# Optimization experiments

Hardware: AMD Instinct MI355X
Metric: run time of the kernel (lower is better)

Reference implementation:

```python
import jax, jax.numpy as jnp
import numpy as np

N_NODES = 50000
E_EDGES = 800000
NODE_DIM = 64
HID = 128


def _leaky(x):
    return jnp.where(x > 0, x, 0.2 * x)


def _gat_conv(x, W, a_src, a_dst, b, src, dst, heads, out_ch, concat):
    # x: [N, in]; W: [in, heads*out]; a_src/a_dst: [heads, out]
    N = x.shape[0]
    h = (x @ W).reshape(N, heads, out_ch)            # [N, H, C]
    s = (h * a_src[None]).sum(-1)                    # [N, H]
    d = (h * a_dst[None]).sum(-1)                    # [N, H]
    e = _leaky(s[src] + d[dst])                      # [E, H]
    m = jax.ops.segment_max(e, dst, num_segments=N)  # segment softmax (stable)
    ex = jnp.exp(e - m[dst])
    denom = jax.ops.segment_sum(ex, dst, num_segments=N)
    alpha = ex / denom[dst]                          # [E, H] (self-loops -> denom>0)
    out = jax.ops.segment_sum(h[src] * alpha[..., None], dst, num_segments=N)
    out = out.reshape(N, heads * out_ch) if concat else out.mean(axis=1)
    return out + b


def setup_inputs() -> dict:
    key = jax.random.key(0)
    ks = jax.random.split(key, 16)
    sc = 0.1
    inp = {
        "x": jax.random.normal(ks[0], (N_NODES, NODE_DIM), jnp.float32),
        "edge_index": jax.random.randint(ks[1], (2, E_EDGES), 0, N_NODES, jnp.int64),
        "fc_w": jax.random.normal(ks[2], (NODE_DIM, HID), jnp.float32) * sc,
        "fc_b": jnp.zeros((HID,), jnp.float32),
        "W1": jax.random.normal(ks[3], (HID, 2 * HID), jnp.float32) * sc,
        "asrc1": jax.random.normal(ks[4], (2, HID), jnp.float32) * sc,
        "adst1": jax.random.normal(ks[5], (2, HID), jnp.float32) * sc,
        "b1": jnp.zeros((2 * HID,), jnp.float32),
        "Wm": jax.random.normal(ks[6], (4, 2 * HID, 2 * HID), jnp.float32) * sc,
        "asrcm": jax.random.normal(ks[7], (4, 2, HID), jnp.float32) * sc,
        "adstm": jax.random.normal(ks[8], (4, 2, HID), jnp.float32) * sc,
        "bm": jnp.zeros((4, 2 * HID), jnp.float32),
        "W6": jax.random.normal(ks[9], (2 * HID, HID), jnp.float32) * sc,
        "asrc6": jax.random.normal(ks[10], (1, HID), jnp.float32) * sc,
        "adst6": jax.random.normal(ks[11], (1, HID), jnp.float32) * sc,
        "b6": jnp.zeros((HID,), jnp.float32),
    }
    return inp


def reference(x, edge_index, fc_w, fc_b, W1, asrc1, adst1, b1,
              Wm, asrcm, adstm, bm, W6, asrc6, adst6, b6):
    N = x.shape[0]
    loops = jnp.arange(N, dtype=edge_index.dtype)
    src = jnp.concatenate([edge_index[0], loops])  # add_self_loops=True (PyG default)
    dst = jnp.concatenate([edge_index[1], loops])

    out = jax.nn.relu(x @ fc_w + fc_b)
    out = _gat_conv(out, W1, asrc1, adst1, b1, src, dst, 2, HID, True)
    for i in range(4):
        out = _gat_conv(out, Wm[i], asrcm[i], adstm[i], bm[i], src, dst, 2, HID, True)
    out = _gat_conv(out, W6, asrc6, adst6, b6, src, dst, 1, HID, True)
    return out
```

## Files before the change

kernel.cpp:

```cpp
#include <hip/hip_runtime.h>
#include <cstdint>
#include <cstddef>

#define NN 50000
#define EE 800000
#define ET 850000

typedef unsigned short ushort_t;
typedef unsigned int uint_t;
using frag_ab = __attribute__((ext_vector_type(8))) short;
using f32x4   = __attribute__((ext_vector_type(4))) float;
using f32x2   = __attribute__((ext_vector_type(2))) float;

__device__ inline ushort_t f2b(float x) {
  union { float f; unsigned int u; } c; c.f = x;
  unsigned int u = c.u;
  u += 0x7fffu + ((u >> 16) & 1u);
  return (ushort_t)(u >> 16);
}
__device__ inline float b2f(uint_t u) {
  union { unsigned int u; float f; } c; c.u = u << 16;
  return c.f;
}
__device__ inline f32x2 unp2(uint_t u) {
  union { uint_t u; float f; } lo, hi;
  lo.u = u << 16; hi.u = u & 0xffff0000u;
  f32x2 r; r.x = lo.f; r.y = hi.f; return r;
}

__device__ inline void gload16(const ushort_t* g, ushort_t* l) {
  __builtin_amdgcn_global_load_lds(
      (const __attribute__((address_space(1))) unsigned int*)g,
      (__attribute__((address_space(3))) unsigned int*)l, 16, 0, 0);
}

__global__ __launch_bounds__(256) void k_count(const int* __restrict__ edge,
                                               int* __restrict__ counts) {
  int e = blockIdx.x * 256 + threadIdx.x;
  if (e >= ET) return;
  int dd = (e < EE) ? edge[EE + e] : (e - EE);
  atomicAdd(&counts[dd], 1);
}

__global__ __launch_bounds__(1024) void k_scan1(const int* __restrict__ counts,
                                                int* __restrict__ scn,
                                                int* __restrict__ bsum) {
  __shared__ int tmp[1024];
  int tid = threadIdx.x;
  int idx = blockIdx.x * 1024 + tid;
  int v = (idx < NN) ? counts[idx] : 0;
  tmp[tid] = v;
  __syncthreads();
  for (int o = 1; o < 1024; o <<= 1) {
    int u = (tid >= o) ? tmp[tid - o] : 0;
    __syncthreads();
    tmp[tid] += u;
    __syncthreads();
  }
  if (idx < NN) scn[idx] = tmp[tid] - v;
  if (tid == 1023) bsum[blockIdx.x] = tmp[1023];
}

__global__ __launch_bounds__(64) void k_scan2(const int* __restrict__ bsum,
                                              int* __restrict__ boff) {
  int l = threadIdx.x;
  const int NB = (NN + 1023) / 1024;
  int v = (l < NB) ? bsum[l] : 0;
  int own = v;
  for (int o = 1; o < 64; o <<= 1) {
    int u = __shfl_up(v, o);
    if (l >= o) v += u;
  }
  if (l < NB) boff[l] = v - own;
}

__global__ __launch_bounds__(1024) void k_scan3(const int* __restrict__ scn,
                                                const int* __restrict__ boff,
                                                int* __restrict__ row_ptr,
                                                int* __restrict__ cursor) {
  int idx = blockIdx.x * 1024 + threadIdx.x;
  if (idx < NN) {
    int v = scn[idx] + boff[blockIdx.x];
    row_ptr[idx] = v;
    cursor[idx] = v;
  }
  if (idx == 0) row_ptr[NN] = ET;
}

__global__ __launch_bounds__(256) void k_fill(const int* __restrict__ edge,
                                              int* __restrict__ cursor,
                                              int* __restrict__ col_src) {
  int e = blockIdx.x * 256 + threadIdx.x;
  if (e >= ET) return;
  int ss, dd;
  if (e < EE) { ss = edge[e]; dd = edge[EE + e]; }
  else        { ss = dd = e - EE; }
  int pos = atomicAdd(&cursor[dd], 1);
  col_src[pos] = ss;
}

__global__ __launch_bounds__(256) void k_prep_w(const float* __restrict__ fc_w,
                                                const float* __restrict__ W1,
                                                const float* __restrict__ Wm,
                                                const float* __restrict__ W6,
                                                ushort_t* __restrict__ fcWt,
                                                ushort_t* __restrict__ W1t,
                                                ushort_t* __restrict__ Wmt,
                                                ushort_t* __restrict__ W6t) {
  int i = blockIdx.x * 256 + threadIdx.x;
  if (i < 128 * 64) { int n = i >> 6, k = i & 63; fcWt[i] = f2b(fc_w[k * 128 + n]); return; }
  i -= 128 * 64;
  if (i < 256 * 128) { int n = i >> 7, k = i & 127; W1t[i] = f2b(W1[k * 256 + n]); return; }
  i -= 256 * 128;
  if (i < 4 * 256 * 256) {
    int l = i >> 16, r2 = i & 65535, n = r2 >> 8, k = r2 & 255;
    Wmt[i] = f2b(Wm[(size_t)l * 65536 + k * 256 + n]); return;
  }
  i -= 4 * 256 * 256;
  if (i < 128 * 256) { int n = i >> 8, k = i & 255; W6t[i] = f2b(W6[k * 128 + n]); return; }
}

__global__ __launch_bounds__(256) void k_gemm_f32(const float* __restrict__ A,
                                                  const ushort_t* __restrict__ Bt,
                                                  ushort_t* __restrict__ C,
                                                  int M, int K, int Nc,
                                                  const float* __restrict__ bias) {
  __shared__ ushort_t As[128 * 40];
  __shared__ ushort_t Bs[128 * 40];
  int row0 = blockIdx.x * 128;
  int col0 = blockIdx.y * 128;
  int t = threadIdx.x;
  int lane = t & 63, w = t >> 6;
  int wr = w >> 1, wc = w & 1;
  int r = lane & 15, kg = lane >> 4;

  f32x4 acc[4][4];
#pragma unroll
  for (int m = 0; m < 4; ++m)
#pragma unroll
    for (int n = 0; n < 4; ++n) acc[m][n] = (f32x4){0.f, 0.f, 0.f, 0.f};

  for (int k0 = 0; k0 < K; k0 += 32) {
    __syncthreads();
#pragma unroll
    for (int rep = 0; rep < 4; ++rep) {
      int c = t + rep * 256;
      int row = c >> 3, kc = c & 7;
      int grow = row0 + row;
      if (grow < M) {
        float4 v = *(const float4*)&A[(size_t)grow * K + k0 + kc * 4];
        ushort4 u;
        u.x = f2b(v.x); u.y = f2b(v.y); u.z = f2b(v.z); u.w = f2b(v.w);
        *(ushort4*)&As[row * 40 + kc * 4] = u;
      }
    }
#pragma unroll
    for (int rep = 0; rep < 2; ++rep) {
      int c = t + rep * 256;
      int row = c >> 2, kc = c & 3;
      uint4 v = *(const uint4*)&Bt[(size_t)(col0 + row) * K + k0 + kc * 8];
      *(uint4*)&Bs[row * 40 + kc * 8] = v;
    }
    __syncthreads();

    frag_ab a[4], b[4];
#pragma unroll
    for (int m = 0; m < 4; ++m)
      a[m] = *(const frag_ab*)&As[(wr * 64 + m * 16 + r) * 40 + kg * 8];
#pragma unroll
    for (int n = 0; n < 4; ++n)
      b[n] = *(const frag_ab*)&Bs[(wc * 64 + n * 16 + r) * 40 + kg * 8];
#pragma unroll
    for (int m = 0; m < 4; ++m)
#pragma unroll
      for (int n = 0; n < 4; ++n)
        acc[m][n] = __builtin_amdgcn_mfma_f32_16x16x32_bf16(a[m], b[n], acc[m][n], 0, 0, 0);
  }

#pragma unroll
  for (int m = 0; m < 4; ++m) {
    int gr0 = row0 + wr * 64 + m * 16 + kg * 4;
#pragma unroll
    for (int q = 0; q < 4; ++q) {
      int grow = gr0 + q;
      if (grow >= M) continue;
#pragma unroll
      for (int n = 0; n < 4; ++n) {
        int gcol = col0 + wc * 64 + n * 16 + r;
        float val = acc[m][n][q] + bias[gcol];
        val = fmaxf(val, 0.f);
        C[(size_t)grow * Nc + gcol] = f2b(val);
      }
    }
  }
}

__global__ __launch_bounds__(256) void k_gemm64(const ushort_t* __restrict__ A,
                                                const ushort_t* __restrict__ Bt,
                                                ushort_t* __restrict__ C,
                                                int M, int K, int Nc,
                                                const float* __restrict__ a_src,
                                                const float* __restrict__ a_dst,
                                                float* __restrict__ sbuf,
                                                float* __restrict__ dbuf,
                                                int H) {
  __shared__ __align__(16) char smem[34816];
  ushort_t* As = (ushort_t*)smem;
  ushort_t* Bs = (ushort_t*)(smem + 16384);
  float (*sdred)[2][2] = (float (*)[2][2])(smem + 32768);
  int row0 = blockIdx.x * 128;
  int col0 = blockIdx.y * 128;
  int t = threadIdx.x;
  int lane = t & 63, w = t >> 6;
  int wr = w >> 1, wc = w & 1;
  int r = lane & 15, kg = lane >> 4;

  f32x4 acc[4][4];
#pragma unroll
  for (int m = 0; m < 4; ++m)
#pragma unroll
    for (int n = 0; n < 4; ++n) acc[m][n] = (f32x4){0.f, 0.f, 0.f, 0.f};

  for (int k0 = 0; k0 < K; k0 += 64) {
    __syncthreads();
#pragma unroll
    for (int i = 0; i < 4; ++i) {
      int c = w * 4 + i;
      int b = c * 1024 + lane * 16;
      int row = b >> 7;
      int ks = ((b >> 4) & 7) ^ (row & 7);
      const ushort_t* ga = A + (size_t)(row0 + row) * K + k0 + ks * 8;
      if (row0 + row < M) gload16(ga, &As[c * 512]);
      const ushort_t* gb = Bt + (size_t)(col0 + row) * K + k0 + ks * 8;
      gload16(gb, &Bs[c * 512]);
    }
    __syncthreads();

#pragma unroll
    for (int kk = 0; kk < 2; ++kk) {
      frag_ab af[4], bf[4];
#pragma unroll
      for (int m = 0; m < 4; ++m) {
        int row = wr * 64 + m * 16 + r;
        int byte = row * 128 + ((kk * 64 + kg * 16) ^ ((row & 7) << 4));
        af[m] = *(const frag_ab*)((const char*)As + byte);
      }
#pragma unroll
      for (int n = 0; n < 4; ++n) {
        int row = wc * 64 + n * 16 + r;
        int byte = row * 128 + ((kk * 64 + kg * 16) ^ ((row & 7) << 4));
        bf[n] = *(const frag_ab*)((const char*)Bs + byte);
      }
#pragma unroll
      for (int m = 0; m < 4; ++m)
#pragma unroll
        for (int n = 0; n < 4; ++n)
          acc[m][n] = __builtin_amdgcn_mfma_f32_16x16x32_bf16(af[m], bf[n], acc[m][n], 0, 0, 0);
    }
  }

  int head = blockIdx.y;
  float as_[4], ad_[4];
#pragma unroll
  for (int n = 0; n < 4; ++n) {
    int cloc = wc * 64 + n * 16 + r;
    as_[n] = a_src[head * 128 + cloc];
    ad_[n] = a_dst[head * 128 + cloc];
  }

  __syncthreads();
  char* ct = smem;

#pragma unroll
  for (int m = 0; m < 4; ++m) {
#pragma unroll
    for (int q = 0; q < 4; ++q) {
      int row_loc = wr * 64 + m * 16 + kg * 4 + q;
      int grow = row0 + row_loc;
      float ps = 0.f, pd = 0.f;
      int sw = ((row_loc >> 2) & 3) << 5;
      if (grow < M) {
#pragma unroll
        for (int n = 0; n < 4; ++n) {
          int col = wc * 64 + n * 16 + r;
          float val = acc[m][n][q];
          ps += val * as_[n]; pd += val * ad_[n];
          *(ushort_t*)(ct + row_loc * 256 + ((col * 2) ^ sw)) = f2b(val);
        }
      }
#pragma unroll
      for (int o = 1; o < 16; o <<= 1) {
        ps += __shfl_xor(ps, o);
        pd += __shfl_xor(pd, o);
      }
      if (r == 0) { sdred[row_loc][wc][0] = ps; sdred[row_loc][wc][1] = pd; }
    }
  }
  __syncthreads();

  {
    int sub = t & 7;
    int rbase = t >> 3;
#pragma unroll
    for (int p = 0; p < 4; ++p) {
      int row = p * 32 + rbase;
      int grow = row0 + row;
      if (grow < M) {
        int sw = ((row >> 2) & 3) << 5;
        uint4 v0 = *(const uint4*)(ct + row * 256 + ((sub * 32) ^ sw));
        uint4 v1 = *(const uint4*)(ct + row * 256 + (((sub * 32) ^ sw) + 16));
        *(uint4*)&C[(size_t)grow * Nc + col0 + sub * 16] = v0;
        *(uint4*)&C[(size_t)grow * Nc + col0 + sub * 16 + 8] = v1;
      }
    }
  }

  {
    int row = t >> 1, which = t & 1;
    int grow = row0 + row;
    if (grow < M) {
      float v = sdred[row][0][which] + sdred[row][1][which];
      float* dst = which ? dbuf : sbuf;
      dst[(size_t)grow * H + head] = v;
    }
  }
}

__global__ __launch_bounds__(256) void k_agg2(const ushort_t* __restrict__ h2,
                                              const float* __restrict__ s,
                                              const float* __restrict__ dv,
                                              const int* __restrict__ row_ptr,
                                              const int* __restrict__ col_src,
                                              const float* __restrict__ bias,
                                              uint4* __restrict__ out) {
  int wid = threadIdx.x >> 6, l = threadIdx.x & 63;
  int n = blockIdx.x * 4 + wid;
  if (n >= NN) return;
  int beg = row_ptr[n], end = row_ptr[n + 1];
  int deg = end - beg;
  float2 tdn = ((const float2*)dv)[n];
  float dn0 = tdn.x, dn1 = tdn.y;
  int hw = l >> 5, lh = l & 31, hd = lh >> 4;
  const char* hb = (const char*)h2 + lh * 16;

  f32x2 A0 = {0.f, 0.f}, A1 = {0.f, 0.f}, A2 = {0.f, 0.f}, A3 = {0.f, 0.f};
  float d0, d1;

  if (deg <= 64) {
    int srcv = 0; float x0 = -1e30f, x1 = -1e30f;
    if (l < deg) {
      srcv = col_src[beg + l];
      float2 sv = ((const float2*)s)[srcv];
      x0 = sv.x + dn0; x0 = x0 > 0.f ? x0 : 0.2f * x0;
      x1 = sv.y + dn1; x1 = x1 > 0.f ? x1 : 0.2f * x1;
    }
    int offv = srcv << 9;

    uint4 P[12];
#pragma unroll
    for (int i = 0; i < 12; ++i)
      P[i] = *(const uint4*)(hb + __shfl(offv, 2 * i + hw));

    float m0 = x0, m1 = x1;
#pragma unroll
    for (int o = 1; o < 64; o <<= 1) {
      m0 = fmaxf(m0, __shfl_xor(m0, o));
      m1 = fmaxf(m1, __shfl_xor(m1, o));
    }
    float p0 = __expf(x0 - m0), p1 = __expf(x1 - m1);
    d0 = p0; d1 = p1;
#pragma unroll
    for (int o = 1; o < 64; o <<= 1) {
      d0 += __shfl_xor(d0, o);
      d1 += __shfl_xor(d1, o);
    }

#pragma unroll
    for (int i = 0; i < 12; ++i) {
      int ep = 2 * i + hw;
      float pa0 = __shfl(p0, ep);
      float pa1 = __shfl(p1, ep);
      float pa = hd ? pa1 : pa0;
      f32x2 pp = {pa, pa};
      A0 = __builtin_elementwise_fma(unp2(P[i].x), pp, A0);
      A1 = __builtin_elementwise_fma(unp2(P[i].y), pp, A1);
      A2 = __builtin_elementwise_fma(unp2(P[i].z), pp, A2);
      A3 = __builtin_elementwise_fma(unp2(P[i].w), pp, A3);
    }
    for (int e = 24; e < deg; e += 8) {
#pragma unroll
      for (int i = 0; i < 4; ++i) {
        int ep = e + 2 * i + hw;
        int off = __shfl(offv, ep);
        float pa0 = __shfl(p0, ep);
        float pa1 = __shfl(p1, ep);
        float pa = hd ? pa1 : pa0;
        uint4 v = *(const uint4*)(hb + off);
        f32x2 pp = {pa, pa};
        A0 = __builtin_elementwise_fma(unp2(v.x), pp, A0);
        A1 = __builtin_elementwise_fma(unp2(v.y), pp, A1);
        A2 = __builtin_elementwise_fma(unp2(v.z), pp, A2);
        A3 = __builtin_elementwise_fma(unp2(v.w), pp, A3);
      }
    }
  } else {
    float m0 = -1e30f, m1 = -1e30f;
    d0 = 0.f; d1 = 0.f;
    for (int e = beg + l; e < end; e += 64) {
      int src = col_src[e];
      float2 sv = ((const float2*)s)[src];
      float x0 = sv.x + dn0; x0 = x0 > 0.f ? x0 : 0.2f * x0;
      if (x0 > m0) { d0 = d0 * __expf(m0 - x0) + 1.f; m0 = x0; } else d0 += __expf(x0 - m0);
      float x1 = sv.y + dn1; x1 = x1 > 0.f ? x1 : 0.2f * x1;
      if (x1 > m1) { d1 = d1 * __expf(m1 - x1) + 1.f; m1 = x1; } else d1 += __expf(x1 - m1);
    }
#pragma unroll
    for (int o = 1; o < 64; o <<= 1) {
      float mo = __shfl_xor(m0, o), dno = __shfl_xor(d0, o);
      float M2 = fmaxf(m0, mo);
      d0 = d0 * __expf(m0 - M2) + dno * __expf(mo - M2);
      m0 = M2;
      mo = __shfl_xor(m1, o); dno = __shfl_xor(d1, o);
      M2 = fmaxf(m1, mo);
      d1 = d1 * __expf(m1 - M2) + dno * __expf(mo - M2);
      m1 = M2;
    }
    for (int c = beg; c < end; c += 64) {
      int cnt = min(64, end - c);
      int srcv = 0; float x0 = -1e30f, x1 = -1e30f;
      if (l < cnt) {
        srcv = col_src[c + l];
        float2 sv = ((const float2*)s)[srcv];
        x0 = sv.x + dn0; x0 = x0 > 0.f ? x0 : 0.2f * x0;
        x1 = sv.y + dn1; x1 = x1 > 0.f ? x1 : 0.2f * x1;
      }
      float p0 = __expf(x0 - m0), p1 = __expf(x1 - m1);
      int offv = srcv << 9;
      for (int e = 0; e < cnt; e += 8) {
#pragma unroll
        for (int i = 0; i < 4; ++i) {
          int ep = e + 2 * i + hw;
          int off = __shfl(offv, ep);
          float pa0 = __shfl(p0, ep);
          float pa1 = __shfl(p1, ep);
          float pa = hd ? pa1 : pa0;
          uint4 v = *(const uint4*)(hb + off);
          f32x2 pp = {pa, pa};
          A0 = __builtin_elementwise_fma(unp2(v.x), pp, A0);
          A1 = __builtin_elementwise_fma(unp2(v.y), pp, A1);
          A2 = __builtin_elementwise_fma(unp2(v.z), pp, A2);
          A3 = __builtin_elementwise_fma(unp2(v.w), pp, A3);
        }
      }
    }
  }

  A0.x += __shfl_xor(A0.x, 32); A0.y += __shfl_xor(A0.y, 32);
  A1.x += __shfl_xor(A1.x, 32); A1.y += __shfl_xor(A1.y, 32);
  A2.x += __shfl_xor(A2.x, 32); A2.y += __shfl_xor(A2.y, 32);
  A3.x += __shfl_xor(A3.x, 32); A3.y += __shfl_xor(A3.y, 32);

  if (hw == 0) {
    float dh = hd ? d1 : d0;
    float inv = 1.f / dh;
    float4 b0 = ((const float4*)bias)[2 * lh];
    float4 b1 = ((const float4*)bias)[2 * lh + 1];
    uint4 ov;
    ov.x = (uint_t)f2b(A0.x * inv + b0.x) | ((uint_t)f2b(A0.y * inv + b0.y) << 16);
    ov.y = (uint_t)f2b(A1.x * inv + b0.z) | ((uint_t)f2b(A1.y * inv + b0.w) << 16);
    ov.z = (uint_t)f2b(A2.x * inv + b1.x) | ((uint_t)f2b(A2.y * inv + b1.y) << 16);
    ov.w = (uint_t)f2b(A3.x * inv + b1.z) | ((uint_t)f2b(A3.y * inv + b1.w) << 16);
    out[(size_t)n * 32 + lh] = ov;
  }
}

__global__ __launch_bounds__(256) void k_agg1(const ushort_t* __restrict__ h2,
                                              const float* __restrict__ s,
                                              const float* __restrict__ dv,
                                              const int* __restrict__ row_ptr,
                                              const int* __restrict__ col_src,
                                              const float* __restrict__ bias,
                                              float* __restrict__ out) {
  int wid = threadIdx.x >> 6, l = threadIdx.x & 63;
  int n = blockIdx.x * 4 + wid;
  if (n >= NN) return;
  int beg = row_ptr[n], end = row_ptr[n + 1];
  int deg = end - beg;
  float dn0 = dv[n];
  int hw = l >> 4, lh = l & 15;
  const char* hb = (const char*)h2 + lh * 16;

  f32x2 A0 = {0.f, 0.f}, A1 = {0.f, 0.f}, A2 = {0.f, 0.f}, A3 = {0.f, 0.f};
  float d0;

  if (deg <= 64) {
    int srcv = 0; float x0 = -1e30f;
    if (l < deg) {
      srcv = col_src[beg + l];
      x0 = s[srcv] + dn0; x0 = x0 > 0.f ? x0 : 0.2f * x0;
    }
    int offv = srcv << 8;

    uint4 P[6];
#pragma unroll
    for (int i = 0; i < 6; ++i)
      P[i] = *(const uint4*)(hb + __shfl(offv, 4 * i + hw));

    float m0 = x0;
#pragma unroll
    for (int o = 1; o < 64; o <<= 1) m0 = fmaxf(m0, __shfl_xor(m0, o));
    float p0 = __expf(x0 - m0);
    d0 = p0;
#pragma unroll
    for (int o = 1; o < 64; o <<= 1) d0 += __shfl_xor(d0, o);

#pragma unroll
    for (int i = 0; i < 6; ++i) {
      float pa = __shfl(p0, 4 * i + hw);
      f32x2 pp = {pa, pa};
      A0 = __builtin_elementwise_fma(unp2(P[i].x), pp, A0);
      A1 = __builtin_elementwise_fma(unp2(P[i].y), pp, A1);
      A2 = __builtin_elementwise_fma(unp2(P[i].z), pp, A2);
      A3 = __builtin_elementwise_fma(unp2(P[i].w), pp, A3);
    }
    for (int e = 24; e < deg; e += 8) {
#pragma unroll
      for (int i = 0; i < 2; ++i) {
        int ep = e + 4 * i + hw;
        int off = __shfl(offv, ep);
        float pa = __shfl(p0, ep);
        uint4 v = *(const uint4*)(hb + off);
        f32x2 pp = {pa, pa};
        A0 = __builtin_elementwise_fma(unp2(v.x), pp, A0);
        A1 = __builtin_elementwise_fma(unp2(v.y), pp, A1);
        A2 = __builtin_elementwise_fma(unp2(v.z), pp, A2);
        A3 = __builtin_elementwise_fma(unp2(v.w), pp, A3);
      }
    }
  } else {
    float m0 = -1e30f;
    d0 = 0.f;
    for (int e = beg + l; e < end; e += 64) {
      float x0 = s[col_src[e]] + dn0;
      x0 = x0 > 0.f ? x0 : 0.2f * x0;
      if (x0 > m0) { d0 = d0 * __expf(m0 - x0) + 1.f; m0 = x0; } else d0 += __expf(x0 - m0);
    }
#pragma unroll
    for (int o = 1; o < 64; o <<= 1) {
      float mo = __shfl_xor(m0, o), dno = __shfl_xor(d0, o);
      float M2 = fmaxf(m0, mo);
      d0 = d0 * __expf(m0 - M2) + dno * __expf(mo - M2);
      m0 = M2;
    }
    for (int c = beg; c < end; c += 64) {
      int cnt = min(64, end - c);
      int srcv = 0; float x0 = -1e30f;
      if (l < cnt) {
        srcv = col_src[c + l];
        x0 = s[srcv] + dn0; x0 = x0 > 0.f ? x0 : 0.2f * x0;
      }
      float p0 = __expf(x0 - m0);
      int offv = srcv << 8;
      for (int e = 0; e < cnt; e += 8) {
#pragma unroll
        for (int i = 0; i < 2; ++i) {
          int ep = e + 4 * i + hw;
          int off = __shfl(offv, ep);
          float pa = __shfl(p0, ep);
          uint4 v = *(const uint4*)(hb + off);
          f32x2 pp = {pa, pa};
          A0 = __builtin_elementwise_fma(unp2(v.x), pp, A0);
          A1 = __builtin_elementwise_fma(unp2(v.y), pp, A1);
          A2 = __builtin_elementwise_fma(unp2(v.z), pp, A2);
          A3 = __builtin_elementwise_fma(unp2(v.w), pp, A3);
        }
      }
    }
  }

#pragma unroll
  for (int o = 16; o < 64; o <<= 1) {
    A0.x += __shfl_xor(A0.x, o); A0.y += __shfl_xor(A0.y, o);
    A1.x += __shfl_xor(A1.x, o); A1.y += __shfl_xor(A1.y, o);
    A2.x += __shfl_xor(A2.x, o); A2.y += __shfl_xor(A2.y, o);
    A3.x += __shfl_xor(A3.x, o); A3.y += __shfl_xor(A3.y, o);
  }
  if (hw == 0) {
    float inv = 1.f / d0;
    float4 b0 = ((const float4*)bias)[2 * lh];
    float4 b1 = ((const float4*)bias)[2 * lh + 1];
    float4 o0 = make_float4(A0.x * inv + b0.x, A0.y * inv + b0.y,
                            A1.x * inv + b0.z, A1.y * inv + b0.w);
    float4 o1 = make_float4(A2.x * inv + b1.x, A2.y * inv + b1.y,
                            A3.x * inv + b1.z, A3.y * inv + b1.w);
    ((float4*)out)[(size_t)n * 32 + 2 * lh] = o0;
    ((float4*)out)[(size_t)n * 32 + 2 * lh + 1] = o1;
  }
}

extern "C" void kernel_launch(void* const* d_in, const int* in_sizes, int n_in,
                              void* d_out, int out_size, void* d_ws, size_t ws_size,
                              hipStream_t stream) {
  const float* x     = (const float*)d_in[0];
  const int*   edge  = (const int*)d_in[1];
  const float* fc_w  = (const float*)d_in[2];
  const float* fc_b  = (const float*)d_in[3];
  const float* W1    = (const float*)d_in[4];
  const float* asrc1 = (const float*)d_in[5];
  const float* adst1 = (const float*)d_in[6];
  const float* b1    = (const float*)d_in[7];
  const float* Wm    = (const float*)d_in[8];
  const float* asrcm = (const float*)d_in[9];
  const float* adstm = (const float*)d_in[10];
  const float* bm    = (const float*)d_in[11];
  const float* W6    = (const float*)d_in[12];
  const float* asrc6 = (const float*)d_in[13];
  const float* adst6 = (const float*)d_in[14];
  const float* b6    = (const float*)d_in[15];

  char* w = (char*)d_ws;
  size_t off = 0;
  auto carve = [&](size_t bytes) -> char* {
    char* p = w + off;
    off = (off + bytes + 255) & ~(size_t)255;
    return p;
  };
  ushort_t* feat0 = (ushort_t*)carve((size_t)NN * 256 * 2);
  ushort_t* feat1 = (ushort_t*)carve((size_t)NN * 256 * 2);
  ushort_t* hbuf  = (ushort_t*)carve((size_t)NN * 256 * 2);
  float* sbuf   = (float*)carve((size_t)NN * 2 * 4);
  float* dbuf   = (float*)carve((size_t)NN * 2 * 4);
  ushort_t* fcWt = (ushort_t*)carve((size_t)128 * 64 * 2);
  ushort_t* W1t  = (ushort_t*)carve((size_t)256 * 128 * 2);
  ushort_t* Wmt  = (ushort_t*)carve((size_t)4 * 256 * 256 * 2);
  ushort_t* W6t  = (ushort_t*)carve((size_t)128 * 256 * 2);
  int* counts   = (int*)carve((size_t)NN * 4);
  int* row_ptr  = (int*)carve((size_t)(NN + 1) * 4);
  int* cursor   = (int*)carve((size_t)NN * 4);
  int* col_src  = (int*)carve((size_t)ET * 4);
  int* scn      = (int*)carve((size_t)NN * 4);
  int* bsum     = (int*)carve((size_t)64 * 4);
  int* boff     = (int*)carve((size_t)64 * 4);
  (void)ws_size;

  k_prep_w<<<(335872 + 255) / 256, 256, 0, stream>>>(fc_w, W1, Wm, W6, fcWt, W1t, Wmt, W6t);

  hipMemsetAsync(counts, 0, (size_t)NN * 4, stream);
  int eb = (ET + 255) / 256;
  const int NB = (NN + 1023) / 1024;
  k_count<<<eb, 256, 0, stream>>>(edge, counts);
  k_scan1<<<NB, 1024, 0, stream>>>(counts, scn, bsum);
  k_scan2<<<1, 64, 0, stream>>>(bsum, boff);
  k_scan3<<<NB, 1024, 0, stream>>>(scn, boff, row_ptr, cursor);
  k_fill<<<eb, 256, 0, stream>>>(edge, cursor, col_src);

  dim3 g1((NN + 127) / 128, 1), g2((NN + 127) / 128, 2);
  int ab = (NN + 3) / 4;

  auto gat = [&](const ushort_t* in, int K, const ushort_t* Wt, const float* a_s,
                 const float* a_d, const float* bias, void* outp, int H) {
    k_gemm64<<<(H == 2 ? g2 : g1), 256, 0, stream>>>(
        in, Wt, hbuf, NN, K, H * 128, a_s, a_d, sbuf, dbuf, H);
    if (H == 2)
      k_agg2<<<ab, 256, 0, stream>>>(hbuf, sbuf, dbuf, row_ptr, col_src, bias, (uint4*)outp);
    else
      k_agg1<<<ab, 256, 0, stream>>>(hbuf, sbuf, dbuf, row_ptr, col_src, bias, (float*)outp);
  };

  k_gemm_f32<<<g1, 256, 0, stream>>>(x, fcWt, feat0, NN, 64, 128, fc_b);

  gat(feat0, 128, W1t, asrc1, adst1, b1, feat1, 2);

  const ushort_t* cur = feat1;
  ushort_t* nxt = feat0;
  for (int i = 0; i < 4; ++i) {
    gat(cur, 256, Wmt + (size_t)i * 256 * 256, asrcm + (size_t)i * 2 * 128,
        adstm + (size_t)i * 2 * 128, bm + (size_t)i * 256, nxt, 2);
    const ushort_t* tmp = cur;
    cur = nxt;
    nxt = (ushort_t*)tmp;
  }

  gat(cur, 256, W6t, asrc6, adst6, b6, d_out, 1);
}
```

Baseline: 578.5 us.

## Process two destination nodes per wavefront in two-head aggregation

k_agg2 now assigns a pair of adjacent nodes to each wavefront. It prefetches 10 neighbor rows for each node before running both softmax reductions, which gives more independent gathers in flight and halves the grid size. Tail iterations now mask out-of-range lanes by zeroing the weight instead of relying on shuffle indices past the degree, and k_agg1 gets the same fix. In exchange, register pressure rises (20 prefetched uint4 plus more scalars), which may lower occupancy, and the prefetch depth per node drops from 12 to 10.

After: 594.9 us. +2.8%, slower.

```diff
diff --git a/kernel.cpp b/kernel.cpp
--- a/kernel.cpp
+++ b/kernel.cpp
@@ -334,67 +334,82 @@
                                               const float* __restrict__ bias,
                                               uint4* __restrict__ out) {
   int wid = threadIdx.x >> 6, l = threadIdx.x & 63;
-  int n = blockIdx.x * 4 + wid;
-  if (n >= NN) return;
-  int beg = row_ptr[n], end = row_ptr[n + 1];
-  int deg = end - beg;
-  float2 tdn = ((const float2*)dv)[n];
-  float dn0 = tdn.x, dn1 = tdn.y;
+  int pr = blockIdx.x * 4 + wid;
+  int n0 = pr * 2;
+  if (n0 >= NN) return;
+  int n1 = n0 + 1;
   int hw = l >> 5, lh = l & 31, hd = lh >> 4;
   const char* hb = (const char*)h2 + lh * 16;
 
-  f32x2 A0 = {0.f, 0.f}, A1 = {0.f, 0.f}, A2 = {0.f, 0.f}, A3 = {0.f, 0.f};
-  float d0, d1;
-
-  if (deg <= 64) {
-    int srcv = 0; float x0 = -1e30f, x1 = -1e30f;
-    if (l < deg) {
-      srcv = col_src[beg + l];
-      float2 sv = ((const float2*)s)[srcv];
-      x0 = sv.x + dn0; x0 = x0 > 0.f ? x0 : 0.2f * x0;
-      x1 = sv.y + dn1; x1 = x1 > 0.f ? x1 : 0.2f * x1;
-    }
-    int offv = srcv << 9;
-
-    uint4 P[12];
-#pragma unroll
-    for (int i = 0; i < 12; ++i)
-      P[i] = *(const uint4*)(hb + __shfl(offv, 2 * i + hw));
-
-    float m0 = x0, m1 = x1;
+  int beg0 = row_ptr[n0], end0 = row_ptr[n0 + 1];
+  int end1 = row_ptr[n1 + 1];
+  int beg1 = end0;
+  int deg0 = end0 - beg0, deg1 = end1 - beg1;
+  float2 q0 = ((const float2*)dv)[n0];
+  float2 q1 = ((const float2*)dv)[n1];
+
+  if (deg0 <= 64 && deg1 <= 64) {
+    int s0v = 0, s1v = 0;
+    float x00 = -1e30f, x01 = -1e30f, x10 = -1e30f, x11 = -1e30f;
+    if (l < deg0) {
+      s0v = col_src[beg0 + l];
+      float2 sv = ((const float2*)s)[s0v];
+      x00 = sv.x + q0.x; x00 = x00 > 0.f ? x00 : 0.2f * x00;
+      x01 = sv.y + q0.y; x01 = x01 > 0.f ? x01 : 0.2f * x01;
+    }
+    if (l < deg1) {
+      s1v = col_src[beg1 + l];
+      float2 sv = ((const float2*)s)[s1v];
+      x10 = sv.x + q1.x; x10 = x10 > 0.f ? x10 : 0.2f * x10;
+      x11 = sv.y + q1.y; x11 = x11 > 0.f ? x11 : 0.2f * x11;
+    }
+    int o0 = s0v << 9, o1 = s1v << 9;
+
+    uint4 P0[10], P1[10];
+#pragma unroll
+    for (int i = 0; i < 10; ++i)
+      P0[i] = *(const uint4*)(hb + __shfl(o0, 2 * i + hw));
+#pragma unroll
+    for (int i = 0; i < 10; ++i)
+      P1[i] = *(const uint4*)(hb + __shfl(o1, 2 * i + hw));
+
+    float m00 = x00, m01 = x01, m10 = x10, m11 = x11;
 #pragma unroll
     for (int o = 1; o < 64; o <<= 1) {
-      m0 = fmaxf(m0, __shfl_xor(m0, o));
-      m1 = fmaxf(m1, __shfl_xor(m1, o));
-    }
-    float p0 = __expf(x0 - m0), p1 = __expf(x1 - m1);
-    d0 = p0; d1 = p1;
+      m00 = fmaxf(m00, __shfl_xor(m00, o));
+      m01 = fmaxf(m01, __shfl_xor(m01, o));
+      m10 = fmaxf(m10, __shfl_xor(m10, o));
+      m11 = fmaxf(m11, __shfl_xor(m11, o));
+    }
+    float p00 = __expf(x00 - m00), p01 = __expf(x01 - m01);
+    float p10 = __expf(x10 - m10), p11 = __expf(x11 - m11);
+    float d00 = p00, d01 = p01, d10 = p10, d11 = p11;
 #pragma unroll
     for (int o = 1; o < 64; o <<= 1) {
-      d0 += __shfl_xor(d0, o);
-      d1 += __shfl_xor(d1, o);
-    }
-
-#pragma unroll
-    for (int i = 0; i < 12; ++i) {
+      d00 += __shfl_xor(d00, o); d01 += __shfl_xor(d01, o);
+      d10 += __shfl_xor(d10, o); d11 += __shfl_xor(d11, o);
+    }
+
+    f32x2 A0 = {0.f, 0.f}, A1 = {0.f, 0.f}, A2 = {0.f, 0.f}, A3 = {0.f, 0.f};
+#pragma unroll
+    for (int i = 0; i < 10; ++i) {
       int ep = 2 * i + hw;
-      float pa0 = __shfl(p0, ep);
-      float pa1 = __shfl(p1, ep);
+      float pa0 = __shfl(p00, ep), pa1 = __shfl(p01, ep);
       float pa = hd ? pa1 : pa0;
       f32x2 pp = {pa, pa};
-      A0 = __builtin_elementwise_fma(unp2(P[i].x), pp, A0);
-      A1 = __builtin_elementwise_fma(unp2(P[i].y), pp, A1);
-      A2 = __builtin_elementwise_fma(unp2(P[i].z), pp, A2);
-      A3 = __builtin_elementwise_fma(unp2(P[i].w), pp, A3);
-    }
-    for (int e = 24; e < deg; e += 8) {
+      A0 = __builtin_elementwise_fma(unp2(P0[i].x), pp, A0);
+      A1 = __builtin_elementwise_fma(unp2(P0[i].y), pp, A1);
+      A2 = __builtin_elementwise_fma(unp2(P0[i].z), pp, A2);
+      A3 = __builtin_elementwise_fma(unp2(P0[i].w), pp, A3);
+    }
+    for (int e = 20; e < deg0; e += 8) {
 #pragma unroll
       for (int i = 0; i < 4; ++i) {
         int ep = e + 2 * i + hw;
-        int off = __shfl(offv, ep);
-        float pa0 = __shfl(p0, ep);
-        float pa1 = __shfl(p1, ep);
+        int off = __shfl(o0, ep & 63);
+        float pa0 = __shfl(p00, ep & 63), pa1 = __shfl(p01, ep & 63);
         float pa = hd ? pa1 : pa0;
+        if (ep >= deg0) pa = 0.f;
         uint4 v = *(const uint4*)(hb + off);
         f32x2 pp = {pa, pa};
         A0 = __builtin_elementwise_fma(unp2(v.x), pp, A0);
@@ -403,74 +418,138 @@
         A3 = __builtin_elementwise_fma(unp2(v.w), pp, A3);
       }
     }
+    A0.x += __shfl_xor(A0.x, 32); A0.y += __shfl_xor(A0.y, 32);
+    A1.x += __shfl_xor(A1.x, 32); A1.y += __shfl_xor(A1.y, 32);
+    A2.x += __shfl_xor(A2.x, 32); A2.y += __shfl_xor(A2.y, 32);
+    A3.x += __shfl_xor(A3.x, 32); A3.y += __shfl_xor(A3.y, 32);
+    if (hw == 0) {
+      float inv = 1.f / (hd ? d01 : d00);
+      float4 b0 = ((const float4*)bias)[2 * lh];
+      float4 b1 = ((const float4*)bias)[2 * lh + 1];
+      uint4 ov;
+      ov.x = (uint_t)f2b(A0.x * inv + b0.x) | ((uint_t)f2b(A0.y * inv + b0.y) << 16);
+      ov.y = (uint_t)f2b(A1.x * inv + b0.z) | ((uint_t)f2b(A1.y * inv + b0.w) << 16);
+      ov.z = (uint_t)f2b(A2.x * inv + b1.x) | ((uint_t)f2b(A2.y * inv + b1.y) << 16);
+      ov.w = (uint_t)f2b(A3.x * inv + b1.z) | ((uint_t)f2b(A3.y * inv + b1.w) << 16);
+      out[(size_t)n0 * 32 + lh] = ov;
+    }
+
+    A0 = (f32x2){0.f, 0.f}; A1 = (f32x2){0.f, 0.f};
+    A2 = (f32x2){0.f, 0.f}; A3 = (f32x2){0.f, 0.f};
+#pragma unroll
+    for (int i = 0; i < 10; ++i) {
+      int ep = 2 * i + hw;
+      float pa0 = __shfl(p10, ep), pa1 = __shfl(p11, ep);
+      float pa = hd ? pa1 : pa0;
+      f32x2 pp = {pa, pa};
+      A0 = __builtin_elementwise_fma(unp2(P1[i].x), pp, A0);
+      A1 = __builtin_elementwise_fma(unp2(P1[i].y), pp, A1);
+      A2 = __builtin_elementwise_fma(unp2(P1[i].z), pp, A2);
+      A3 = __builtin_elementwise_fma(unp2(P1[i].w), pp, A3);
+    }
+    for (int e = 20; e < deg1; e += 8) {
+#pragma unroll
+      for (int i = 0; i < 4; ++i) {
+        int ep = e + 2 * i + hw;
+        int off = __shfl(o1, ep & 63);
+        float pa0 = __shfl(p10, ep & 63), pa1 = __shfl(p11, ep & 63);
+        float pa = hd ? pa1 : pa0;
+        if (ep >= deg1) pa = 0.f;
+        uint4 v = *(const uint4*)(hb + off);
+        f32x2 pp = {pa, pa};
+        A0 = __builtin_elementwise_fma(unp2(v.x), pp, A0);
+        A1 = __builtin_elementwise_fma(unp2(v.y), pp, A1);
+        A2 = __builtin_elementwise_fma(unp2(v.z), pp, A2);
+        A3 = __builtin_elementwise_fma(unp2(v.w), pp, A3);
+      }
+    }
+    A0.x += __shfl_xor(A0.x, 32); A0.y += __shfl_xor(A0.y, 32);
+    A1.x += __shfl_xor(A1.x, 32); A1.y += __shfl_xor(A1.y, 32);
+    A2.x += __shfl_xor(A2.x, 32); A2.y += __shfl_xor(A2.y, 32);
+    A3.x += __shfl_xor(A3.x, 32); A3.y += __shfl_xor(A3.y, 32);
+    if (hw == 0) {
+      float inv = 1.f / (hd ? d11 : d10);
+      float4 b0 = ((const float4*)bias)[2 * lh];
+      float4 b1 = ((const float4*)bias)[2 * lh + 1];
+      uint4 ov;
+      ov.x = (uint_t)f2b(A0.x * inv + b0.x) | ((uint_t)f2b(A0.y * inv + b0.y) << 16);
+      ov.y = (uint_t)f2b(A1.x * inv + b0.z) | ((uint_t)f2b(A1.y * inv + b0.w) << 16);
+      ov.z = (uint_t)f2b(A2.x * inv + b1.x) | ((uint_t)f2b(A2.y * inv + b1.y) << 16);
+      ov.w = (uint_t)f2b(A3.x * inv + b1.z) | ((uint_t)f2b(A3.y * inv + b1.w) << 16);
+      out[(size_t)n1 * 32 + lh] = ov;
+    }
   } else {
-    float m0 = -1e30f, m1 = -1e30f;
-    d0 = 0.f; d1 = 0.f;
-    for (int e = beg + l; e < end; e += 64) {
-      int src = col_src[e];
-      float2 sv = ((const float2*)s)[src];
-      float x0 = sv.x + dn0; x0 = x0 > 0.f ? x0 : 0.2f * x0;
-      if (x0 > m0) { d0 = d0 * __expf(m0 - x0) + 1.f; m0 = x0; } else d0 += __expf(x0 - m0);
-      float x1 = sv.y + dn1; x1 = x1 > 0.f ? x1 : 0.2f * x1;
-      if (x1 > m1) { d1 = d1 * __expf(m1 - x1) + 1.f; m1 = x1; } else d1 += __expf(x1 - m1);
-    }
-#pragma unroll
-    for (int o = 1; o < 64; o <<= 1) {
-      float mo = __shfl_xor(m0, o), dno = __shfl_xor(d0, o);
-      float M2 = fmaxf(m0, mo);
-      d0 = d0 * __expf(m0 - M2) + dno * __expf(mo - M2);
-      m0 = M2;
-      mo = __shfl_xor(m1, o); dno = __shfl_xor(d1, o);
-      M2 = fmaxf(m1, mo);
-      d1 = d1 * __expf(m1 - M2) + dno * __expf(mo - M2);
-      m1 = M2;
-    }
-    for (int c = beg; c < end; c += 64) {
-      int cnt = min(64, end - c);
-      int srcv = 0; float x0 = -1e30f, x1 = -1e30f;
-      if (l < cnt) {
-        srcv = col_src[c + l];
-        float2 sv = ((const float2*)s)[srcv];
-        x0 = sv.x + dn0; x0 = x0 > 0.f ? x0 : 0.2f * x0;
-        x1 = sv.y + dn1; x1 = x1 > 0.f ? x1 : 0.2f * x1;
-      }
-      float p0 = __expf(x0 - m0), p1 = __expf(x1 - m1);
-      int offv = srcv << 9;
-      for (int e = 0; e < cnt; e += 8) {
-#pragma unroll
-        for (int i = 0; i < 4; ++i) {
-          int ep = e + 2 * i + hw;
-          int off = __shfl(offv, ep);
-          float pa0 = __shfl(p0, ep);
-          float pa1 = __shfl(p1, ep);
-          float pa = hd ? pa1 : pa0;
-          uint4 v = *(const uint4*)(hb + off);
-          f32x2 pp = {pa, pa};
-          A0 = __builtin_elementwise_fma(unp2(v.x), pp, A0);
-          A1 = __builtin_elementwise_fma(unp2(v.y), pp, A1);
-          A2 = __builtin_elementwise_fma(unp2(v.z), pp, A2);
-          A3 = __builtin_elementwise_fma(unp2(v.w), pp, A3);
+#pragma unroll 1
+    for (int which = 0; which < 2; ++which) {
+      int n = which ? n1 : n0;
+      int beg = which ? beg1 : beg0;
+      int end = which ? end1 : end0;
+      float dn0 = which ? q1.x : q0.x, dn1 = which ? q1.y : q0.y;
+      f32x2 A0 = {0.f, 0.f}, A1 = {0.f, 0.f}, A2 = {0.f, 0.f}, A3 = {0.f, 0.f};
+      float m0 = -1e30f, m1 = -1e30f, d0 = 0.f, d1 = 0.f;
+      for (int e = beg + l; e < end; e += 64) {
+        int src = col_src[e];
+        float2 sv = ((const float2*)s)[src];
+        float x0 = sv.x + dn0; x0 = x0 > 0.f ? x0 : 0.2f * x0;
+        if (x0 > m0) { d0 = d0 * __expf(m0 - x0) + 1.f; m0 = x0; } else d0 += __expf(x0 - m0);
+        float x1 = sv.y + dn1; x1 = x1 > 0.f ? x1 : 0.2f * x1;
+        if (x1 > m1) { d1 = d1 * __expf(m1 - x1) + 1.f; m1 = x1; } else d1 += __expf(x1 - m1);
+      }
+#pragma unroll
+      for (int o = 1; o < 64; o <<= 1) {
+        float mo = __shfl_xor(m0, o), dno = __shfl_xor(d0, o);
+        float M2 = fmaxf(m0, mo);
+        d0 = d0 * __expf(m0 - M2) + dno * __expf(mo - M2);
+        m0 = M2;
+        mo = __shfl_xor(m1, o); dno = __shfl_xor(d1, o);
+        M2 = fmaxf(m1, mo);
+        d1 = d1 * __expf(m1 - M2) + dno * __expf(mo - M2);
+        m1 = M2;
+      }
+      for (int c = beg; c < end; c += 64) {
+        int cnt = min(64, end - c);
+        int srcv = 0; float x0 = -1e30f, x1 = -1e30f;
+        if (l < cnt) {
+          srcv = col_src[c + l];
+          float2 sv = ((const float2*)s)[srcv];
+          x0 = sv.x + dn0; x0 = x0 > 0.f ? x0 : 0.2f * x0;
+          x1 = sv.y + dn1; x1 = x1 > 0.f ? x1 : 0.2f * x1;
         }
-      }
-    }
-  }
-
-  A0.x += __shfl_xor(A0.x, 32); A0.y += __shfl_xor(A0.y, 32);
-  A1.x += __shfl_xor(A1.x, 32); A1.y += __shfl_xor(A1.y, 32);
-  A2.x += __shfl_xor(A2.x, 32); A2.y += __shfl_xor(A2.y, 32);
-  A3.x += __shfl_xor(A3.x, 32); A3.y += __shfl_xor(A3.y, 32);
-
-  if (hw == 0) {
-    float dh = hd ? d1 : d0;
-    float inv = 1.f / dh;
-    float4 b0 = ((const float4*)bias)[2 * lh];
-    float4 b1 = ((const float4*)bias)[2 * lh + 1];
-    uint4 ov;
-    ov.x = (uint_t)f2b(A0.x * inv + b0.x) | ((uint_t)f2b(A0.y * inv + b0.y) << 16);
-    ov.y = (uint_t)f2b(A1.x * inv + b0.z) | ((uint_t)f2b(A1.y * inv + b0.w) << 16);
-    ov.z = (uint_t)f2b(A2.x * inv + b1.x) | ((uint_t)f2b(A2.y * inv + b1.y) << 16);
-    ov.w = (uint_t)f2b(A3.x * inv + b1.z) | ((uint_t)f2b(A3.y * inv + b1.w) << 16);
-    out[(size_t)n * 32 + lh] = ov;
+        float p0 = __expf(x0 - m0), p1 = __expf(x1 - m1);
+        int offv = srcv << 9;
+        for (int e = 0; e < cnt; e += 8) {
+#pragma unroll
+          for (int i = 0; i < 4; ++i) {
+            int ep = e + 2 * i + hw;
+            int off = __shfl(offv, ep & 63);
+            float pa0 = __shfl(p0, ep & 63), pa1 = __shfl(p1, ep & 63);
+            float pa = hd ? pa1 : pa0;
+            if (ep >= cnt) pa = 0.f;
+            uint4 v = *(const uint4*)(hb + off);
+            f32x2 pp = {pa, pa};
+            A0 = __builtin_elementwise_fma(unp2(v.x), pp, A0);
+            A1 = __builtin_elementwise_fma(unp2(v.y), pp, A1);
+            A2 = __builtin_elementwise_fma(unp2(v.z), pp, A2);
+            A3 = __builtin_elementwise_fma(unp2(v.w), pp, A3);
+          }
+        }
+      }
+      A0.x += __shfl_xor(A0.x, 32); A0.y += __shfl_xor(A0.y, 32);
+      A1.x += __shfl_xor(A1.x, 32); A1.y += __shfl_xor(A1.y, 32);
+      A2.x += __shfl_xor(A2.x, 32); A2.y += __shfl_xor(A2.y, 32);
+      A3.x += __shfl_xor(A3.x, 32); A3.y += __shfl_xor(A3.y, 32);
+      if (hw == 0) {
+        float inv = 1.f / (hd ? d1 : d0);
+        float4 b0 = ((const float4*)bias)[2 * lh];
+        float4 b1 = ((const float4*)bias)[2 * lh + 1];
+        uint4 ov;
+        ov.x = (uint_t)f2b(A0.x * inv + b0.x) | ((uint_t)f2b(A0.y * inv + b0.y) << 16);
+        ov.y = (uint_t)f2b(A1.x * inv + b0.z) | ((uint_t)f2b(A1.y * inv + b0.w) << 16);
+        ov.z = (uint_t)f2b(A2.x * inv + b1.x) | ((uint_t)f2b(A2.y * inv + b1.y) << 16);
+        ov.w = (uint_t)f2b(A3.x * inv + b1.z) | ((uint_t)f2b(A3.y * inv + b1.w) << 16);
+        out[(size_t)n * 32 + lh] = ov;
+      }
+    }
   }
 }
 
@@ -565,8 +644,9 @@
 #pragma unroll
         for (int i = 0; i < 2; ++i) {
           int ep = e + 4 * i + hw;
-          int off = __shfl(offv, ep);
-          float pa = __shfl(p0, ep);
+          int off = __shfl(offv, ep & 63);
+          float pa = __shfl(p0, ep & 63);
+          if (ep >= cnt) pa = 0.f;
           uint4 v = *(const uint4*)(hb + off);
           f32x2 pp = {pa, pa};
           A0 = __builtin_elementwise_fma(unp2(v.x), pp, A0);
@@ -656,13 +736,14 @@
 
   dim3 g1((NN + 127) / 128, 1), g2((NN + 127) / 128, 2);
   int ab = (NN + 3) / 4;
+  int ab2 = (NN / 2 + 3) / 4;
 
   auto gat = [&](const ushort_t* in, int K, const ushort_t* Wt, const float* a_s,
                  const float* a_d, const float* bias, void* outp, int H) {
     k_gemm64<<<(H == 2 ? g2 : g1), 256, 0, stream>>>(
         in, Wt, hbuf, NN, K, H * 128, a_s, a_d, sbuf, dbuf, H);
     if (H == 2)
-      k_agg2<<<ab, 256, 0, stream>>>(hbuf, sbuf, dbuf, row_ptr, col_src, bias, (uint4*)outp);
+      k_agg2<<<ab2, 256, 0, stream>>>(hbuf, sbuf, dbuf, row_ptr, col_src, bias, (uint4*)outp);
     else
       k_agg1<<<ab, 256, 0, stream>>>(hbuf, sbuf, dbuf, row_ptr, col_src, bias, (float*)outp);
   };
```
